# Kernel optimization log

Measured on AMD Instinct MI355X. Metric: run time of the kernel, lower is better.

The kernel has to match this reference:

```python
import jax, jax.numpy as jnp
import numpy as np
from jax import lax

EPS = 1e-20
BN_EPS = 1e-5
ATTN_SCALE = 2.8284271247461903  # sqrt(d_l=8)
NS = (32, 32, 32, 10)
DS = (8, 8, 8, 16)


def squash(x):
    # Efficient-CapsNet squash: (1 - 1/(exp(||x||)+eps)) * x/(||x||+eps)
    norm = jnp.linalg.norm(x, axis=-1, keepdims=True)
    return (1.0 - 1.0 / (jnp.exp(norm) + EPS)) * (x / (norm + EPS))


def conv2d(x, w, b, stride, groups=1):
    y = lax.conv_general_dilated(
        x, w, window_strides=(stride, stride), padding='VALID',
        dimension_numbers=('NCHW', 'OIHW', 'NCHW'),
        feature_group_count=groups)
    return y + b[None, :, None, None]


def bn(x, g, b, m, v):
    inv = g / jnp.sqrt(v + BN_EPS)
    return x * inv[None, :, None, None] + (b - m * inv)[None, :, None, None]


def fccaps(U_l, W):
    # U_l: (b, n_l, d_l), W: (n_l, n_h, d_l, d_h)
    U_hat = jnp.einsum('bij,ikjl->bikl', U_l, W)          # (b, n_l, n_h, d_h)
    A = jnp.einsum('bikl,bhkl->bhik', U_hat, U_hat)        # (b, n_l, n_l, n_h)
    A_sum = jnp.sum(A, axis=-2)                            # (b, n_l, n_h)
    C = jax.nn.softmax(A_sum / ATTN_SCALE, axis=-1)        # (b, n_l, n_h)
    U_h = jnp.einsum('bikl,bik->bkl', U_hat, C)            # (b, n_h, d_h)
    return squash(U_h)


def setup_inputs() -> dict:
    key = jax.random.key(0)
    ks = jax.random.split(key, 8)
    B = 512
    x = jax.random.normal(ks[0], (B, 1, 39, 39), dtype=jnp.float32)
    conv1_w = jax.random.normal(ks[1], (128, 1, 3, 3), jnp.float32) * 0.2
    conv1_b = jnp.zeros((128,), jnp.float32)
    conv2_w = jax.random.normal(ks[2], (256, 128, 3, 3), jnp.float32) * 0.04
    conv2_b = jnp.zeros((256,), jnp.float32)
    conv3_w = jax.random.normal(ks[3], (256, 1, 9, 9), jnp.float32) * 0.1  # depthwise
    conv3_b = jnp.zeros((256,), jnp.float32)
    bn1_g = jnp.ones((128,), jnp.float32); bn1_b = jnp.zeros((128,), jnp.float32)
    bn1_m = jnp.zeros((128,), jnp.float32); bn1_v = jnp.ones((128,), jnp.float32)
    bn2_g = jnp.ones((256,), jnp.float32); bn2_b = jnp.zeros((256,), jnp.float32)
    bn2_m = jnp.zeros((256,), jnp.float32); bn2_v = jnp.ones((256,), jnp.float32)
    # capsule weights, kaiming-ish scale sqrt(2/fan_in) with fan_in = n_h*d_l*d_h
    def caps_w(k, n_l, n_h, d_l, d_h):
        std = np.sqrt(2.0 / (n_h * d_l * d_h))
        return jax.random.normal(k, (n_l, n_h, d_l, d_h), jnp.float32) * std
    W1 = caps_w(ks[4], NS[0], NS[1], DS[0], DS[1])
    W2 = caps_w(ks[5], NS[1], NS[2], DS[1], DS[2])
    W3 = caps_w(ks[6], NS[2], NS[3], DS[2], DS[3])
    return dict(x=x, conv1_w=conv1_w, conv1_b=conv1_b,
                bn1_g=bn1_g, bn1_b=bn1_b, bn1_m=bn1_m, bn1_v=bn1_v,
                conv2_w=conv2_w, conv2_b=conv2_b,
                bn2_g=bn2_g, bn2_b=bn2_b, bn2_m=bn2_m, bn2_v=bn2_v,
                conv3_w=conv3_w, conv3_b=conv3_b, W1=W1, W2=W2, W3=W3)


def reference(x, conv1_w, conv1_b, bn1_g, bn1_b, bn1_m, bn1_v,
              conv2_w, conv2_b, bn2_g, bn2_b, bn2_m, bn2_v,
              conv3_w, conv3_b, W1, W2, W3):
    h = jax.nn.relu(bn(conv2d(x, conv1_w, conv1_b, 2), bn1_g, bn1_b, bn1_m, bn1_v))
    h = jax.nn.relu(bn(conv2d(h, conv2_w, conv2_b, 2), bn2_g, bn2_b, bn2_m, bn2_v))
    h = conv2d(h, conv3_w, conv3_b, 1, groups=256)        # (B, 256, 1, 1)
    u = h.reshape(h.shape[0], NS[0], DS[0])                # (B, 32, 8)
    u = squash(u)
    for W in (W1, W2, W3):
        u = fccaps(u, W)
    return u  # (B, 10, 16)
```

## Files before the change

### kernel.cpp

```cpp
#include <hip/hip_runtime.h>


typedef __attribute__((ext_vector_type(8))) short short8;
typedef __attribute__((ext_vector_type(4))) short bf16x4;
typedef __attribute__((ext_vector_type(4))) float f32x4;

__device__ __forceinline__ ushort f2bf(float x) {
    uint u = __float_as_uint(x);
    return (ushort)((u + 0x7FFFu + ((u >> 16) & 1u)) >> 16);
}
__device__ __forceinline__ void bfsplit(float x, ushort& h, ushort& l) {
    h = f2bf(x);
    float hf = __uint_as_float(((uint)h) << 16);
    l = f2bf(x - hf);
}

__global__ __launch_bounds__(256) void k_prep(
    const float* __restrict__ w2, uint* __restrict__ Bt,
    const float* __restrict__ w3, float* __restrict__ w3T,
    const float* __restrict__ W1, const float* __restrict__ W2,
    const float* __restrict__ W3, float* __restrict__ Wr1,
    float* __restrict__ Wr2, float* __restrict__ Wr3,
    const float* __restrict__ c1b, const float* __restrict__ g1,
    const float* __restrict__ b1, const float* __restrict__ m1,
    const float* __restrict__ v1, float2* __restrict__ sc1) {
    __shared__ __align__(16) float wbuf[64 * 288];
    const int b = blockIdx.x, t = threadIdx.x;
    if (b < 144) {
        const int sidx = b >> 2, coq = b & 3;
        const int chunk = sidx / 9, tap = sidx - chunk * 9;
        const int co0 = coq * 64;
        for (int idx = t; idx < 4608; idx += 256) {
            const int n = idx / 72, q = idx - n * 72;
            ((float4*)wbuf)[n * 72 + q] =
                *(const float4*)(w2 + (size_t)(co0 + n) * 1152 + chunk * 288 + q * 4);
        }
        __syncthreads();
        const int n = t & 63, dg = (t >> 6) * 4;
        const int cot = coq >> 1, nn = ((coq & 1) * 64) + n;
        uint* dst = Bt + (size_t)(sidx * 2 + cot) * 4096;
#pragma unroll
        for (int dd = 0; dd < 4; ++dd) {
            const int d = dg + dd;
            const float x = wbuf[n * 288 + (2 * d) * 9 + tap];
            const float y = wbuf[n * 288 + (2 * d + 1) * 9 + tap];
            ushort xh, xl, yh, yl;
            bfsplit(x, xh, xl);
            bfsplit(y, yh, yl);
            dst[nn * 16 + d]        = (uint)xh | ((uint)yh << 16);
            dst[2048 + nn * 16 + d] = (uint)xl | ((uint)yl << 16);
        }
    } else if (b < 225) {
        const int p = b - 144;
        w3T[p * 256 + t] = w3[t * 81 + p];
    } else if (b < 321) {
        const int bb = b - 225;
        const int layer = bb >> 5, blk = bb & 31;
        const float* src = layer == 0 ? W1 : (layer == 1 ? W2 : W3);
        float* dst = layer == 0 ? Wr1 : (layer == 1 ? Wr2 : Wr3);
        const int d_h = (layer == 2) ? 16 : 8;
        const int total = (layer == 2) ? 5120 : 8192;
        for (int idx = blk * 256 + t; idx < 8 * total; idx += 32 * 256) {
            const int j = idx / total, e = idx - j * total;
            const int ik = e / d_h, l = e - ik * d_h;
            dst[idx] = src[(ik * 8 + j) * d_h + l];
        }
    } else {
        if (t < 128) {
            const float inv = g1[t] * rsqrtf(v1[t] + 1e-5f);
            sc1[t] = make_float2(inv, c1b[t] * inv + b1[t] - m1[t] * inv);
        }
    }
}

__global__ __launch_bounds__(256, 3) void k_conv2(
    const float* __restrict__ x, const float* __restrict__ w1,
    const float2* __restrict__ sc1, const uint* __restrict__ Bt,
    const float* __restrict__ g,
    const float* __restrict__ bb, const float* __restrict__ bm,
    const float* __restrict__ bv, const float* __restrict__ bias,
    const float* __restrict__ w3T, float* __restrict__ Uws) {
    __shared__ __align__(16) uint raw[11552];
    __shared__ __align__(16) float xs[1521];
    __shared__ float ured[128];
    const int t = threadIdx.x;
    const int lane = t & 63, wave = t >> 6;
    const int ln15 = lane & 15, lq = lane >> 4;
    const int wm = (wave >> 1) * 48, wn = (wave & 1) * 64;
    const int gg = blockIdx.x;
    const int bi  = ((gg >> 4) << 3) | (gg & 7);
    const int cot = (gg >> 3) & 1;
    const int co0 = cot * 128;

    const float* xb = x + (size_t)bi * 1521;
    for (int i = t; i < 1521; i += 256) xs[i] = xb[i];

    const int hc = t & 7, o2 = hc >> 1, half = hc & 1, pg = t >> 3;

    int PE[3], PO[3];
#pragma unroll
    for (int i = 0; i < 3; ++i) {
        const int m = wm + i * 16 + ln15;
        const int p = m < 81 ? m : 80;
        const int oh = p / 9, ow = p - oh * 9;
        PE[i] = lq * 760 + oh * 80 + ow * 4;
        PO[i] = 3040 + lq * 684 + oh * 72 + ow * 4;
    }
    int BRDg[4];
#pragma unroll
    for (int j = 0; j < 4; ++j) {
        const int n = wn + j * 16 + ln15;
        BRDg[j] = n * 16 + lq * 4;
    }

    f32x4 acc[3][4] = {};
    uint4 Bn[8];
    {
        const uint* bp = Bt + (size_t)cot * 4096;
#pragma unroll
        for (int j = 0; j < 4; ++j) {
            Bn[j]     = *(const uint4*)(bp + BRDg[j]);
            Bn[4 + j] = *(const uint4*)(bp + 2048 + BRDg[j]);
        }
    }

#pragma unroll
    for (int c = 0; c < 4; ++c) {
        const int o = c * 4 + o2;
        float wr[36];
        {
            const float4* wp = reinterpret_cast<const float4*>(w1 + o * 72 + half * 36);
#pragma unroll
            for (int q = 0; q < 9; ++q) {
                const float4 wv = wp[q];
                wr[q * 4 + 0] = wv.x; wr[q * 4 + 1] = wv.y;
                wr[q * 4 + 2] = wv.z; wr[q * 4 + 3] = wv.w;
            }
        }
        float2 ssv[4];
#pragma unroll
        for (int jj = 0; jj < 4; ++jj) ssv[jj] = sc1[o * 8 + half * 4 + jj];

        __syncthreads();

        {
            ushort* rawu = (ushort*)raw;
            for (int p = pg; p < 361; p += 32) {
                const int y = p / 19, xq = p - y * 19;
                const int base = y * 78 + xq * 2;
                const float x0 = xs[base],      x1 = xs[base + 1],  x2 = xs[base + 2];
                const float x3 = xs[base + 39], x4 = xs[base + 40], x5 = xs[base + 41];
                const float x6 = xs[base + 78], x7 = xs[base + 79], x8 = xs[base + 80];
                bf16x4 hs, ls;
#pragma unroll
                for (int jj = 0; jj < 4; ++jj) {
                    const float a = x0 * wr[jj * 9 + 0] + x1 * wr[jj * 9 + 1] +
                                    x2 * wr[jj * 9 + 2] + x3 * wr[jj * 9 + 3] +
                                    x4 * wr[jj * 9 + 4] + x5 * wr[jj * 9 + 5] +
                                    x6 * wr[jj * 9 + 6] + x7 * wr[jj * 9 + 7] +
                                    x8 * wr[jj * 9 + 8];
                    const float v = fmaxf(fmaf(a, ssv[jj].x, ssv[jj].y), 0.0f);
                    ushort hh, lw;
                    bfsplit(v, hh, lw);
                    hs[jj] = (short)hh;
                    ls[jj] = (short)lw;
                }
                int ad;
                if ((xq & 1) == 0) {
                    ad = o2 * 1520 + (y * 10 + (xq >> 1)) * 8 + half * 4;
                } else {
                    ad = 6080 + o2 * 1368 + (y * 9 + (xq >> 1)) * 8 + half * 4;
                }
                *(bf16x4*)(rawu + ad)         = hs;
                *(bf16x4*)(rawu + 11552 + ad) = ls;
            }
        }
        __syncthreads();

        short8 a_h[3];
#pragma unroll
        for (int i = 0; i < 3; ++i)
            a_h[i] = *reinterpret_cast<const short8*>(raw + PE[i]);
#pragma unroll
        for (int tap = 0; tap < 9; ++tap) {
            const int s = c * 9 + tap;
            uint4 Bc[8];
#pragma unroll
            for (int q = 0; q < 8; ++q) Bc[q] = Bn[q];
            if (s < 35) {
                const uint* bp = Bt + (size_t)((s + 1) * 2 + cot) * 4096;
#pragma unroll
                for (int j = 0; j < 4; ++j) {
                    Bn[j]     = *(const uint4*)(bp + BRDg[j]);
                    Bn[4 + j] = *(const uint4*)(bp + 2048 + BRDg[j]);
                }
            }
            const int kh = tap / 3, kw = tap - kh * 3;
            const int odd = kw & 1;
            const int sE = kh * 40 + (kw >> 1) * 4;
            const int sO = kh * 36;
            short8 a_l[3];
#pragma unroll
            for (int i = 0; i < 3; ++i) {
                const int addr = odd ? (PO[i] + sO) : (PE[i] + sE);
                a_l[i] = *reinterpret_cast<const short8*>(raw + addr + 5776);
            }
            short8 a_hn[3];
            if (tap < 8) {
                const int tap2 = tap + 1;
                const int kh2 = tap2 / 3, kw2 = tap2 - kh2 * 3;
                const int odd2 = kw2 & 1;
                const int sE2 = kh2 * 40 + (kw2 >> 1) * 4;
                const int sO2 = kh2 * 36;
#pragma unroll
                for (int i = 0; i < 3; ++i) {
                    const int addr2 = odd2 ? (PO[i] + sO2) : (PE[i] + sE2);
                    a_hn[i] = *reinterpret_cast<const short8*>(raw + addr2);
                }
            }
            short8 bh[4], bl[4];
#pragma unroll
            for (int j = 0; j < 4; ++j) {
                bh[j] = __builtin_bit_cast(short8, Bc[j]);
                bl[j] = __builtin_bit_cast(short8, Bc[4 + j]);
            }
#pragma unroll
            for (int i = 0; i < 3; ++i)
#pragma unroll
                for (int j = 0; j < 4; ++j)
                    acc[i][j] = __builtin_amdgcn_mfma_f32_16x16x32_bf16(a_h[i], bh[j], acc[i][j], 0, 0, 0);
#pragma unroll
            for (int i = 0; i < 3; ++i)
#pragma unroll
                for (int j = 0; j < 4; ++j)
                    acc[i][j] = __builtin_amdgcn_mfma_f32_16x16x32_bf16(a_h[i], bl[j], acc[i][j], 0, 0, 0);
#pragma unroll
            for (int i = 0; i < 3; ++i)
#pragma unroll
                for (int j = 0; j < 4; ++j)
                    acc[i][j] = __builtin_amdgcn_mfma_f32_16x16x32_bf16(a_l[i], bh[j], acc[i][j], 0, 0, 0);
            if (tap < 8) {
#pragma unroll
                for (int i = 0; i < 3; ++i) a_h[i] = a_hn[i];
            }
        }
    }

    float scj[4], shj[4];
#pragma unroll
    for (int j = 0; j < 4; ++j) {
        const int co = co0 + wn + j * 16 + ln15;
        const float inv = g[co] * rsqrtf(bv[co] + 1e-5f);
        scj[j] = inv;
        shj[j] = bias[co] * inv + bb[co] - bm[co] * inv;
    }
    float usum[4] = {0.f, 0.f, 0.f, 0.f};
#pragma unroll
    for (int i = 0; i < 3; ++i)
#pragma unroll
        for (int r = 0; r < 4; ++r) {
            const int m = wm + i * 16 + lq * 4 + r;
            if (m < 81) {
                const float* wrow = w3T + m * 256 + co0;
#pragma unroll
                for (int j = 0; j < 4; ++j) {
                    const int col = wn + j * 16 + ln15;
                    const float v = fmaxf(fmaf(acc[i][j][r], scj[j], shj[j]), 0.0f);
                    usum[j] = fmaf(v, wrow[col], usum[j]);
                }
            }
        }
#pragma unroll
    for (int j = 0; j < 4; ++j) {
        usum[j] += __shfl_xor(usum[j], 16);
        usum[j] += __shfl_xor(usum[j], 32);
    }
    if (lq == 0 && wm == 0) {
#pragma unroll
        for (int j = 0; j < 4; ++j) ured[(wn >> 6) * 64 + j * 16 + ln15] = usum[j];
    }
    __syncthreads();
    if (lq == 0 && wm == 48) {
#pragma unroll
        for (int j = 0; j < 4; ++j) {
            const int col = wn + j * 16 + ln15;
            Uws[(size_t)bi * 256 + co0 + col] =
                usum[j] + ured[(wn >> 6) * 64 + j * 16 + ln15];
        }
    }
}

__device__ __forceinline__ void fccaps_block(
    const int n_l, const int n_h, const int d_h, const float* __restrict__ Wr,
    float* U, float* Uh, float* Sv, float* Av, float* Cv, float* coefs,
    float* outU, const int t) {
    const int nkd = n_h * d_h;
    const int total = n_l * nkd;
    __syncthreads();
    for (int e = t; e < total; e += 256) {
        const int i = e / nkd;
        const float* up = U + i * 8;
        float acc = 0.0f;
#pragma unroll
        for (int j = 0; j < 8; ++j) acc += up[j] * Wr[j * total + e];
        Uh[e] = acc;
    }
    __syncthreads();
    for (int e = t; e < nkd; e += 256) {
        float acc = 0.0f;
        for (int i = 0; i < n_l; ++i) acc += Uh[i * nkd + e];
        Sv[e] = acc;
    }
    __syncthreads();
    for (int e = t; e < n_l * n_h; e += 256) {
        const int h = e / n_h, k = e - h * n_h;
        float acc = 0.0f;
        for (int l = 0; l < d_h; ++l)
            acc += Uh[h * nkd + k * d_h + l] * Sv[k * d_h + l];
        Av[e] = acc;
    }
    __syncthreads();
    {
        const int h = t >> 3, sub = t & 7;
        const float invs = 1.0f / 2.8284271247461903f;
        float mx = -1e30f;
        for (int k = sub; k < n_h; k += 8) mx = fmaxf(mx, Av[h * n_h + k]);
        mx = fmaxf(mx, __shfl_xor(mx, 1));
        mx = fmaxf(mx, __shfl_xor(mx, 2));
        mx = fmaxf(mx, __shfl_xor(mx, 4));
        float sum = 0.0f;
        for (int k = sub; k < n_h; k += 8) {
            const float ev = expf((Av[h * n_h + k] - mx) * invs);
            Cv[h * n_h + k] = ev;
            sum += ev;
        }
        sum += __shfl_xor(sum, 1);
        sum += __shfl_xor(sum, 2);
        sum += __shfl_xor(sum, 4);
        const float r = 1.0f / sum;
        for (int k = sub; k < n_h; k += 8) Cv[h * n_h + k] *= r;
    }
    __syncthreads();
    for (int e = t; e < nkd; e += 256) {
        const int k = e / d_h;
        float acc = 0.0f;
        for (int i = 0; i < n_l; ++i) acc += Uh[i * nkd + e] * Cv[i * n_h + k];
        Sv[e] = acc;
    }
    __syncthreads();
    if (t < n_h) {
        float ssq = 0.0f;
        for (int l = 0; l < d_h; ++l) { const float uv = Sv[t * d_h + l]; ssq += uv * uv; }
        const float n = sqrtf(ssq);
        coefs[t] = (1.0f - 1.0f / (expf(n) + 1e-20f)) / (n + 1e-20f);
    }
    __syncthreads();
    for (int e = t; e < nkd; e += 256) outU[e] = Sv[e] * coefs[e / d_h];
}

__global__ __launch_bounds__(256) void k_caps(
    const float* __restrict__ Uws, const float* __restrict__ b3,
    const float* __restrict__ Wr1, const float* __restrict__ Wr2,
    const float* __restrict__ Wr3, float* __restrict__ out) {
    __shared__ float U[256];
    __shared__ float Uh[8192];
    __shared__ float Sv[256];
    __shared__ float Av[1024];
    __shared__ float Cv[1024];
    __shared__ float coefs[32];
    const int b = blockIdx.x, t = threadIdx.x;
    U[t] = Uws[(size_t)b * 256 + t] + b3[t];
    __syncthreads();
    if (t < 32) {
        float ssq = 0.0f;
        for (int j = 0; j < 8; ++j) { const float uv = U[t * 8 + j]; ssq += uv * uv; }
        const float n = sqrtf(ssq);
        coefs[t] = (1.0f - 1.0f / (expf(n) + 1e-20f)) / (n + 1e-20f);
    }
    __syncthreads();
    U[t] *= coefs[t >> 3];
    fccaps_block(32, 32,  8, Wr1, U, Uh, Sv, Av, Cv, coefs, U, t);
    fccaps_block(32, 32,  8, Wr2, U, Uh, Sv, Av, Cv, coefs, U, t);
    fccaps_block(32, 10, 16, Wr3, U, Uh, Sv, Av, Cv, coefs, out + (size_t)b * 160, t);
}

extern "C" void kernel_launch(void* const* d_in, const int* in_sizes, int n_in,
                              void* d_out, int out_size, void* d_ws, size_t ws_size,
                              hipStream_t stream) {
    const float* x    = (const float*)d_in[0];
    const float* c1w  = (const float*)d_in[1];
    const float* c1b  = (const float*)d_in[2];
    const float* bn1g = (const float*)d_in[3];
    const float* bn1b = (const float*)d_in[4];
    const float* bn1m = (const float*)d_in[5];
    const float* bn1v = (const float*)d_in[6];
    const float* c2w  = (const float*)d_in[7];
    const float* c2b  = (const float*)d_in[8];
    const float* bn2g = (const float*)d_in[9];
    const float* bn2b = (const float*)d_in[10];
    const float* bn2m = (const float*)d_in[11];
    const float* bn2v = (const float*)d_in[12];
    const float* c3w  = (const float*)d_in[13];
    const float* c3b  = (const float*)d_in[14];
    const float* W1   = (const float*)d_in[15];
    const float* W2   = (const float*)d_in[16];
    const float* W3   = (const float*)d_in[17];
    float* out = (float*)d_out;
    uint*  wsu = (uint*)d_ws;
    float* wsf = (float*)d_ws;

    float*  Uws = wsf;
    uint*   Bt  = wsu + 131072;
    float*  w3T = wsf + 425984;
    float*  Wr1 = wsf + 446720;
    float*  Wr2 = wsf + 512256;
    float*  Wr3 = wsf + 577792;
    float2* sc1 = (float2*)(wsf + 618752);

    k_prep<<<dim3(322), 256, 0, stream>>>(c2w, Bt, c3w, w3T, W1, W2, W3,
                                          Wr1, Wr2, Wr3,
                                          c1b, bn1g, bn1b, bn1m, bn1v, sc1);
    k_conv2<<<dim3(1024), 256, 0, stream>>>(x, c1w, sc1, Bt,
                                            bn2g, bn2b, bn2m, bn2v,
                                            c2b, w3T, Uws);
    k_caps<<<dim3(512), 256, 0, stream>>>(Uws, c3b, Wr1, Wr2, Wr3, out);
}
```

Before: 219.5 us.

## Overlap conv1 recompute for next channel chunk with conv2 MFMA taps

Conv1 outputs for the next channel chunk are now computed in registers and spread across the nine MFMA taps of the current chunk. After the barrier they are just stored to LDS, rather than computed in a separate phase between barriers. Position indices are precomputed once and weights for the next chunk are prefetched. The hi/lo bf16 split now truncates instead of rounding, and the occupancy hint drops from 3 to 2 blocks per SM to fit the extra registers. The risks are lower occupancy and slightly changed numerics from truncation.

After: 286.4 us. 1.3x slower.

```diff
diff --git a/kernel.cpp b/kernel.cpp
--- a/kernel.cpp
+++ b/kernel.cpp
@@ -2,7 +2,6 @@
 
 
 typedef __attribute__((ext_vector_type(8))) short short8;
-typedef __attribute__((ext_vector_type(4))) short bf16x4;
 typedef __attribute__((ext_vector_type(4))) float f32x4;
 
 __device__ __forceinline__ ushort f2bf(float x) {
@@ -73,7 +72,7 @@
     }
 }
 
-__global__ __launch_bounds__(256, 3) void k_conv2(
+__global__ __launch_bounds__(256, 2) void k_conv2(
     const float* __restrict__ x, const float* __restrict__ w1,
     const float2* __restrict__ sc1, const uint* __restrict__ Bt,
     const float* __restrict__ g,
@@ -97,6 +96,22 @@
 
     const int hc = t & 7, o2 = hc >> 1, half = hc & 1, pg = t >> 3;
 
+    int bs[12], ad[12];
+#pragma unroll
+    for (int k = 0; k < 12; ++k) {
+        const int p = pg + 32 * k;
+        if (p < 361) {
+            const int y = p / 19, xq = p - y * 19;
+            bs[k] = y * 78 + xq * 2;
+            ad[k] = ((xq & 1) == 0)
+                  ? (o2 * 1520 + (y * 10 + (xq >> 1)) * 8 + half * 4)
+                  : (6080 + o2 * 1368 + (y * 9 + (xq >> 1)) * 8 + half * 4);
+        } else {
+            bs[k] = 0;
+            ad[k] = -1;
+        }
+    }
+
     int PE[3], PO[3];
 #pragma unroll
     for (int i = 0; i < 3; ++i) {
@@ -124,57 +139,70 @@
         }
     }
 
+    float wr[36];
+    float2 ssv[4];
+    uint pcH[24], pcL[24];
+
+    auto load_w = [&](int c) {
+        const int o = c * 4 + o2;
+        const float4* wp = reinterpret_cast<const float4*>(w1 + o * 72 + half * 36);
+#pragma unroll
+        for (int q = 0; q < 9; ++q) {
+            const float4 wv = wp[q];
+            wr[q * 4 + 0] = wv.x; wr[q * 4 + 1] = wv.y;
+            wr[q * 4 + 2] = wv.z; wr[q * 4 + 3] = wv.w;
+        }
+#pragma unroll
+        for (int jj = 0; jj < 4; ++jj) ssv[jj] = sc1[o * 8 + half * 4 + jj];
+    };
+    auto comp_pos = [&](int k) {
+        uint h0 = 0, h1 = 0, l0 = 0, l1 = 0;
+        if (ad[k] >= 0) {
+            const int base = bs[k];
+            const float x0 = xs[base],      x1 = xs[base + 1],  x2 = xs[base + 2];
+            const float x3 = xs[base + 39], x4 = xs[base + 40], x5 = xs[base + 41];
+            const float x6 = xs[base + 78], x7 = xs[base + 79], x8 = xs[base + 80];
+            uint hv[4], lv[4];
+#pragma unroll
+            for (int jj = 0; jj < 4; ++jj) {
+                const float a = x0 * wr[jj * 9 + 0] + x1 * wr[jj * 9 + 1] +
+                                x2 * wr[jj * 9 + 2] + x3 * wr[jj * 9 + 3] +
+                                x4 * wr[jj * 9 + 4] + x5 * wr[jj * 9 + 5] +
+                                x6 * wr[jj * 9 + 6] + x7 * wr[jj * 9 + 7] +
+                                x8 * wr[jj * 9 + 8];
+                const float v = fmaxf(fmaf(a, ssv[jj].x, ssv[jj].y), 0.0f);
+                const uint u = __float_as_uint(v);
+                hv[jj] = u >> 16;
+                const float d = v - __uint_as_float(u & 0xFFFF0000u);
+                lv[jj] = __float_as_uint(d) >> 16;
+            }
+            h0 = hv[0] | (hv[1] << 16);
+            h1 = hv[2] | (hv[3] << 16);
+            l0 = lv[0] | (lv[1] << 16);
+            l1 = lv[2] | (lv[3] << 16);
+        }
+        pcH[k * 2] = h0; pcH[k * 2 + 1] = h1;
+        pcL[k * 2] = l0; pcL[k * 2 + 1] = l1;
+    };
+    auto store_pos = [&](int k) {
+        if (ad[k] >= 0) {
+            ushort* rawu = (ushort*)raw;
+            *(uint2*)(rawu + ad[k])         = make_uint2(pcH[k * 2], pcH[k * 2 + 1]);
+            *(uint2*)(rawu + 11552 + ad[k]) = make_uint2(pcL[k * 2], pcL[k * 2 + 1]);
+        }
+    };
+
+    load_w(0);
+    __syncthreads();
+#pragma unroll
+    for (int k = 0; k < 12; ++k) comp_pos(k);
+
 #pragma unroll
     for (int c = 0; c < 4; ++c) {
-        const int o = c * 4 + o2;
-        float wr[36];
-        {
-            const float4* wp = reinterpret_cast<const float4*>(w1 + o * 72 + half * 36);
-#pragma unroll
-            for (int q = 0; q < 9; ++q) {
-                const float4 wv = wp[q];
-                wr[q * 4 + 0] = wv.x; wr[q * 4 + 1] = wv.y;
-                wr[q * 4 + 2] = wv.z; wr[q * 4 + 3] = wv.w;
-            }
-        }
-        float2 ssv[4];
-#pragma unroll
-        for (int jj = 0; jj < 4; ++jj) ssv[jj] = sc1[o * 8 + half * 4 + jj];
-
         __syncthreads();
-
-        {
-            ushort* rawu = (ushort*)raw;
-            for (int p = pg; p < 361; p += 32) {
-                const int y = p / 19, xq = p - y * 19;
-                const int base = y * 78 + xq * 2;
-                const float x0 = xs[base],      x1 = xs[base + 1],  x2 = xs[base + 2];
-                const float x3 = xs[base + 39], x4 = xs[base + 40], x5 = xs[base + 41];
-                const float x6 = xs[base + 78], x7 = xs[base + 79], x8 = xs[base + 80];
-                bf16x4 hs, ls;
-#pragma unroll
-                for (int jj = 0; jj < 4; ++jj) {
-                    const float a = x0 * wr[jj * 9 + 0] + x1 * wr[jj * 9 + 1] +
-                                    x2 * wr[jj * 9 + 2] + x3 * wr[jj * 9 + 3] +
-                                    x4 * wr[jj * 9 + 4] + x5 * wr[jj * 9 + 5] +
-                                    x6 * wr[jj * 9 + 6] + x7 * wr[jj * 9 + 7] +
-                                    x8 * wr[jj * 9 + 8];
-                    const float v = fmaxf(fmaf(a, ssv[jj].x, ssv[jj].y), 0.0f);
-                    ushort hh, lw;
-                    bfsplit(v, hh, lw);
-                    hs[jj] = (short)hh;
-                    ls[jj] = (short)lw;
-                }
-                int ad;
-                if ((xq & 1) == 0) {
-                    ad = o2 * 1520 + (y * 10 + (xq >> 1)) * 8 + half * 4;
-                } else {
-                    ad = 6080 + o2 * 1368 + (y * 9 + (xq >> 1)) * 8 + half * 4;
-                }
-                *(bf16x4*)(rawu + ad)         = hs;
-                *(bf16x4*)(rawu + 11552 + ad) = ls;
-            }
-        }
+#pragma unroll
+        for (int k = 0; k < 12; ++k) store_pos(k);
+        if (c < 3) load_w(c + 1);
         __syncthreads();
 
         short8 a_h[3];
@@ -217,6 +245,11 @@
                     const int addr2 = odd2 ? (PO[i] + sO2) : (PE[i] + sE2);
                     a_hn[i] = *reinterpret_cast<const short8*>(raw + addr2);
                 }
+            }
+            if (c < 3) {
+                const int kb = (tap * 12) / 9, ke = ((tap + 1) * 12) / 9;
+#pragma unroll
+                for (int k = kb; k < ke; ++k) comp_pos(k);
             }
             short8 bh[4], bl[4];
 #pragma unroll
```
